# Kernel tuning notes

Hardware: AMD Instinct MI355X
Metric: run time of the kernel (lower is better)

Reference implementation:

```python
import jax, jax.numpy as jnp
import numpy as np
import math

NUM_CONVS = 4
GN_GROUPS = 32
GN_EPS = 1e-5
FPN_STRIDES = (8, 16, 32, 64, 128)
PRIOR_PROB = 0.01


def conv3x3(x, w, b):
    # x: [N,C,H,W], w: [O,I,3,3]
    y = jax.lax.conv_general_dilated(
        x, w, window_strides=(1, 1), padding='SAME',
        dimension_numbers=('NCHW', 'OIHW', 'NCHW'))
    return y + b[None, :, None, None]


def group_norm(x, gamma, beta):
    n, c, h, w = x.shape
    xg = x.reshape(n, GN_GROUPS, c // GN_GROUPS, h, w)
    mean = xg.mean(axis=(2, 3, 4), keepdims=True)
    var = xg.var(axis=(2, 3, 4), keepdims=True)
    xn = ((xg - mean) * jax.lax.rsqrt(var + GN_EPS)).reshape(n, c, h, w)
    return xn * gamma[None, :, None, None] + beta[None, :, None, None]


def subnet(x, ws, bs, gws, gbs):
    # NUM_CONVS x (conv3x3 -> GN -> ReLU)
    for i in range(NUM_CONVS):
        x = jax.nn.relu(group_norm(conv3x3(x, ws[i], bs[i]), gws[i], gbs[i]))
    return x


def permute_to_N_HWA_K(x, k):
    n = x.shape[0]
    return x.transpose(0, 2, 3, 1).reshape(n, -1, k)


def setup_inputs() -> dict:
    key = jax.random.key(0)
    ks = jax.random.split(key, 16)
    C, K = 256, 80
    feats = {
        'p3': jax.random.normal(ks[0], (1, C, 80, 80), jnp.float32),
        'p4': jax.random.normal(ks[1], (1, C, 40, 40), jnp.float32),
        'p5': jax.random.normal(ks[2], (1, C, 20, 20), jnp.float32),
        'p6': jax.random.normal(ks[3], (1, C, 10, 10), jnp.float32),
        'p7': jax.random.normal(ks[4], (1, C, 5, 5), jnp.float32),
    }
    std = 0.01
    bias_value = -math.log((1 - PRIOR_PROB) / PRIOR_PROB)
    params = {
        'cls_w': std * jax.random.normal(ks[5], (NUM_CONVS, C, C, 3, 3), jnp.float32),
        'cls_b': jnp.zeros((NUM_CONVS, C), jnp.float32),
        'cls_gn_w': jnp.ones((NUM_CONVS, C), jnp.float32),
        'cls_gn_b': jnp.zeros((NUM_CONVS, C), jnp.float32),
        'box_w': std * jax.random.normal(ks[6], (NUM_CONVS, C, C, 3, 3), jnp.float32),
        'box_b': jnp.zeros((NUM_CONVS, C), jnp.float32),
        'box_gn_w': jnp.ones((NUM_CONVS, C), jnp.float32),
        'box_gn_b': jnp.zeros((NUM_CONVS, C), jnp.float32),
        'score_w': std * jax.random.normal(ks[7], (K, C, 3, 3), jnp.float32),
        'score_b': jnp.full((K,), bias_value, jnp.float32),
        'pred_w': std * jax.random.normal(ks[8], (4, C, 3, 3), jnp.float32),
        'pred_b': jnp.zeros((4,), jnp.float32),
        'iou_w': std * jax.random.normal(ks[9], (1, C, 3, 3), jnp.float32),
        'iou_b': jnp.zeros((1,), jnp.float32),
        'scales': jnp.ones((5,), jnp.float32),
    }
    return {**feats, **params}


def reference(p3, p4, p5, p6, p7,
              cls_w, cls_b, cls_gn_w, cls_gn_b,
              box_w, box_b, box_gn_w, box_gn_b,
              score_w, score_b, pred_w, pred_b, iou_w, iou_b, scales):
    features = [p3, p4, p5, p6, p7]
    logits, bbox_reg, ious = [], [], []
    for l, feat in enumerate(features):
        c = subnet(feat, cls_w, cls_b, cls_gn_w, cls_gn_b)
        b = subnet(feat, box_w, box_b, box_gn_w, box_gn_b)
        logit = conv3x3(c, score_w, score_b)          # [N,80,H,W]
        iou = conv3x3(b, iou_w, iou_b)                # [N,1,H,W]
        bp = conv3x3(b, pred_w, pred_b) * scales[l]   # Scale module
        # norm_reg_targets=True branch
        reg = jax.nn.relu(bp) * FPN_STRIDES[l]        # [N,4,H,W]
        logits.append(permute_to_N_HWA_K(logit, 80))
        bbox_reg.append(permute_to_N_HWA_K(reg, 4))
        ious.append(permute_to_N_HWA_K(iou, 1))
    box_cls = jnp.concatenate(logits, axis=1)    # [N, sumHW, 80]
    box_delta = jnp.concatenate(bbox_reg, axis=1)  # [N, sumHW, 4]
    box_iou = jnp.concatenate(ious, axis=1)      # [N, sumHW, 1]
    # pack into one array for a single output: [N, sumHW, 85]
    return jnp.concatenate([box_cls, box_delta, box_iou], axis=-1)
```

## Files before the change

kernel.cpp:

```cpp
#include <hip/hip_runtime.h>

typedef unsigned short u16;
typedef __attribute__((ext_vector_type(8))) short bf16x8;
typedef __attribute__((ext_vector_type(4))) float f32x4;

#define NLEV 5
#define CCH 256
#define KTOT 2304
#define P_TOT 8525
#define PP_TOT 9165
#define PLS (PP_TOT*64)
#define HSTR 11776

__constant__ int   c_HW[NLEV]     = {6400, 1600, 400, 100, 25};
__constant__ int   c_W[NLEV]      = {80, 40, 20, 10, 5};
__constant__ int   c_off[NLEV]    = {0, 6400, 8000, 8400, 8500};
__constant__ int   c_poff[NLEV]   = {0, 6724, 8488, 8972, 9116};
__constant__ int   c_tls[NLEV+1]  = {0, 50, 65, 71, 73, 74};
__constant__ int   c_ntx[NLEV]    = {5, 3, 2, 1, 1};
__constant__ float c_stridef[NLEV]= {8.f, 16.f, 32.f, 64.f, 128.f};

__device__ __forceinline__ u16 f2bf(float f){
  union { float f; unsigned u; } v; v.f = f;
  unsigned r = v.u + 0x7fffu + ((v.u >> 16) & 1u);
  return (u16)(r >> 16);
}

__device__ __forceinline__ void g2l16(const u16* g, u16* l, int lane){
#if defined(__has_builtin)
#if __has_builtin(__builtin_amdgcn_global_load_lds)
  __builtin_amdgcn_global_load_lds(
      (const __attribute__((address_space(1))) unsigned int*)g,
      (__attribute__((address_space(3))) unsigned int*)l, 16, 0, 0);
  return;
#endif
#endif
  *(uint4*)(l + lane*8) = *(const uint4*)g;
}

#define WAIT_VM4   0x0F74
#define WAIT_VM10  0x0F7A
#define WAIT_VM0   0x0F70
#define WAIT_LGKM0 0xC07F

template<int MODE>
__global__ __launch_bounds__(256, 2) void gemm_conv(
    const u16* __restrict__ Xc, const u16* __restrict__ Xb,
    const u16* __restrict__ Wc, const u16* __restrict__ Wb,
    const float* __restrict__ bc, const float* __restrict__ bb,
    float* __restrict__ Yc, float* __restrict__ Yb,
    float* __restrict__ stats,
    const float* __restrict__ predb, const float* __restrict__ ioub,
    const float* __restrict__ scales, float* __restrict__ out)
{
  __shared__ u16 hB[2*HSTR];
  __shared__ u16 sA[4][2][2048];
  __shared__ float sstat[16][2];

  const int ptile = blockIdx.x;
  const int mtile = (MODE == 0) ? blockIdx.y : 0;
  const int br = blockIdx.z;
  int lv = 0;
  #pragma unroll
  for (int i = 1; i < NLEV; i++) if (ptile >= c_tls[i]) lv = i;
  const int tidx = ptile - c_tls[lv];
  const int ntx = c_ntx[lv];
  const int ty0 = (tidx / ntx) * 8, tx0 = (tidx - (tidx / ntx) * ntx) * 16;
  const int W = c_W[lv], wrow2 = W + 2;

  const int tid = threadIdx.x, wv = tid >> 6, ln = tid & 63;
  const int quad = ln >> 4, l15 = ln & 15;

  const u16* __restrict__ X  = br ? Xb : Xc;
  const u16* __restrict__ WA = br ? Wb : Wc;

  const int ASTR = (MODE == 0) ? 16384 : 8192;
  const u16* abase = WA +
      (size_t)(((MODE == 0) ? mtile*16 : 0) + wv*4) * 512 + ln*8;

  const u16* hptr[6]; int hslab[6];
  #pragma unroll
  for (int i = 0; i < 6; i++) {
    int j = wv + 4*i;
    if (j > 22) j -= 4;
    hslab[i] = j;
    const int item = j*64 + ln;
    int hp = item >> 3; if (hp >= 180) hp -= 180;
    const int g = item & 7;
    const int hy = hp / 18, hx = hp - hy*18;
    const int prow = c_poff[lv] + (ty0 + hy)*wrow2 + tx0 + hx;
    hptr[i] = X + (size_t)prow*64 + ((g ^ (hp & 7)) << 3);
  }

  auto stageH = [&](int plane) {
    u16* dst = &hB[(plane & 1) * HSTR];
    const size_t cof = (size_t)plane * PLS;
    #pragma unroll
    for (int i = 0; i < 6; i++)
      g2l16(hptr[i] + cof, dst + hslab[i]*512, ln);
  };
  auto stageA = [&](int s, int b) {
    const u16* as = abase + (size_t)s * ASTR;
    u16* da = &sA[wv][b][0];
    #pragma unroll
    for (int j = 0; j < 4; j++) g2l16(as + j*512, da + j*512, ln);
  };

  f32x4 acc[2][8];
  #pragma unroll
  for (int i = 0; i < 2; i++)
    #pragma unroll
    for (int j = 0; j < 8; j++) acc[i][j] = (f32x4){0.f, 0.f, 0.f, 0.f};

  if (MODE == 0 && tid < 32) sstat[tid >> 1][tid & 1] = 0.f;

  stageH(0);
  stageH(1);
  stageA(0, 0);
  stageA(4, 1);
  __syncthreads();

  int cc = 0, tap = 0;
  #pragma unroll 1
  for (int t = 0; t < 36; t++) {
    if (t == 10 || t == 19) __builtin_amdgcn_s_waitcnt(WAIT_VM10);
    else if (t == 35)       __builtin_amdgcn_s_waitcnt(WAIT_VM0);
    else                    __builtin_amdgcn_s_waitcnt(WAIT_VM4);
    if (tap == 0 && cc > 0) {
      __builtin_amdgcn_sched_barrier(0);
      __builtin_amdgcn_s_barrier();
      __builtin_amdgcn_sched_barrier(0);
      if (cc < 3) stageH(cc + 1);
    }
    const u16* myA = &sA[wv][t & 1][0];
    const u16* hpl = &hB[(cc & 1) * HSTR];
    const int dh = tap / 3, dw = tap - dh*3;
    bf16x8 af[2][2], bf[2][8];
    #pragma unroll
    for (int sub = 0; sub < 2; sub++) {
      const int q = sub*4 + quad;
      const int swzA = (q ^ (l15 & 7)) * 8;
      #pragma unroll
      for (int mt = 0; mt < 2; mt++)
        af[sub][mt] = *(const bf16x8*)&myA[(mt*16 + l15)*64 + swzA];
      #pragma unroll
      for (int nt = 0; nt < 8; nt++) {
        const int hp = (nt + dh)*18 + l15 + dw;
        bf[sub][nt] = *(const bf16x8*)&hpl[hp*64 + ((q ^ (hp & 7)) << 3)];
      }
    }
    __builtin_amdgcn_s_waitcnt(WAIT_LGKM0);
    if (t < 34) {
      int tap2 = tap + 2, cc2 = cc;
      if (tap2 >= 9) { tap2 -= 9; cc2++; }
      stageA(tap2*4 + cc2, t & 1);
    }
    #pragma unroll
    for (int sub = 0; sub < 2; sub++)
      #pragma unroll
      for (int mt = 0; mt < 2; mt++)
        #pragma unroll
        for (int nt = 0; nt < 8; nt++)
          acc[mt][nt] = __builtin_amdgcn_mfma_f32_16x16x32_bf16(
              af[sub][mt], bf[sub][nt], acc[mt][nt], 0, 0, 0);
    if (++tap == 9) { tap = 0; cc++; }
  }

  const int gx = tx0 + l15;
  if (MODE == 0) {
    const float* __restrict__ bias = br ? bb : bc;
    float* __restrict__ Y = br ? Yb : Yc;
    #pragma unroll
    for (int mt = 0; mt < 2; mt++) {
      const int mloc = wv*32 + mt*16 + quad*4;
      const int mrow = mtile*128 + mloc;
      const f32x4 bv = *(const f32x4*)&bias[mrow];
      float s = 0.f, sq = 0.f;
      #pragma unroll
      for (int nt = 0; nt < 8; nt++) {
        const int gy = ty0 + nt;
        f32x4 v = acc[mt][nt] + bv;
        if (gy < W && gx < W) {
          const size_t n = (size_t)(c_off[lv] + gy*W + gx);
          *(f32x4*)&Y[n*CCH + mrow] = v;
          #pragma unroll
          for (int r = 0; r < 4; r++) { s += v[r]; sq += v[r]*v[r]; }
        }
      }
      #pragma unroll
      for (int o = 1; o < 16; o <<= 1) { s += __shfl_xor(s, o); sq += __shfl_xor(sq, o); }
      if (l15 == 0) {
        const int g = mloc >> 3;
        atomicAdd(&sstat[g][0], s);
        atomicAdd(&sstat[g][1], sq);
      }
    }
    __syncthreads();
    if (tid < 32) {
      const int g = tid >> 1, c = tid & 1;
      atomicAdd(&stats[((br*NLEV + lv)*32 + mtile*16 + g)*2 + c], sstat[g][c]);
    }
  } else {
    const float scl = scales[lv];
    const float stf = c_stridef[lv];
    #pragma unroll
    for (int mt = 0; mt < 2; mt++) {
      const int mr0 = wv*32 + mt*16 + quad*4;
      if (mr0 >= 85) continue;
      #pragma unroll
      for (int nt = 0; nt < 8; nt++) {
        const int gy = ty0 + nt;
        if (gy >= W || gx >= W) continue;
        const size_t n = (size_t)(c_off[lv] + gy*W + gx);
        const f32x4 v = acc[mt][nt];
        #pragma unroll
        for (int r = 0; r < 4; r++) {
          const int m = mr0 + r;
          if (br == 0) {
            if (m < 80) out[n*85 + m] = v[r] + bc[m];
          } else {
            if (m < 4) {
              const float t = (v[r] + predb[m]) * scl;
              out[n*85 + 80 + m] = fmaxf(t, 0.f) * stf;
            } else if (m == 4) {
              out[n*85 + 84] = v[r] + ioub[0];
            }
          }
        }
      }
    }
  }
}

__global__ __launch_bounds__(256) void gn_relu(
    const float* __restrict__ Yc, const float* __restrict__ Yb,
    const float* __restrict__ stats,
    const float* __restrict__ gwc, const float* __restrict__ gbc,
    const float* __restrict__ gwb, const float* __restrict__ gbb,
    u16* __restrict__ Xc, u16* __restrict__ Xb)
{
  const int t = blockIdx.x * 256 + threadIdx.x;
  if (t >= 2 * P_TOT * 32) return;
  const int br = t / (P_TOT * 32);
  const int r  = t - br * (P_TOT * 32);
  const int pg = r >> 5;
  const int c0 = (r & 31) << 3;
  int lv = 0;
  #pragma unroll
  for (int i = 1; i < NLEV; i++) if (pg >= c_off[i]) lv = i;
  const int pl = pg - c_off[lv];
  const int Wl = c_W[lv];
  const int g = c0 >> 3;
  const float* st = &stats[(((size_t)br*NLEV + lv)*32 + g)*2];
  const float cnt = 8.f * (float)c_HW[lv];
  const float mean = st[0] / cnt;
  const float var  = st[1] / cnt - mean*mean;
  const float rstd = rsqrtf(var + 1e-5f);
  const float* Y  = br ? Yb : Yc;
  const float* gw = br ? gwb : gwc;
  const float* gb = br ? gbb : gbc;
  u16* X = br ? Xb : Xc;
  const float* y = &Y[(size_t)pg*CCH + c0];
  const int h = pl / Wl, wi = pl - h*Wl;
  const size_t pidx = (size_t)(c_poff[lv] + (h+1)*(Wl+2) + (wi+1));
  union { u16 u[8]; uint4 v; } pk;
  #pragma unroll
  for (int i = 0; i < 8; i++) {
    const float v = (y[i] - mean)*rstd*gw[c0+i] + gb[c0+i];
    pk.u[i] = f2bf(fmaxf(v, 0.f));
  }
  *(uint4*)&X[(size_t)(c0 >> 6)*PLS + pidx*64 + (c0 & 63)] = pk.v;
}

__global__ __launch_bounds__(256) void feat2bf(
    const float* __restrict__ p3, const float* __restrict__ p4,
    const float* __restrict__ p5, const float* __restrict__ p6,
    const float* __restrict__ p7, u16* __restrict__ X)
{
  const int t = blockIdx.x * 256 + threadIdx.x;
  if (t >= P_TOT * 32) return;
  const int pg = t >> 5, c0 = (t & 31) << 3;
  int lv = 0;
  #pragma unroll
  for (int i = 1; i < NLEV; i++) if (pg >= c_off[i]) lv = i;
  const int pl = pg - c_off[lv];
  const float* src = lv==0 ? p3 : lv==1 ? p4 : lv==2 ? p5 : lv==3 ? p6 : p7;
  const int HW = c_HW[lv], Wl = c_W[lv];
  const int h = pl / Wl, wi = pl - h*Wl;
  const size_t pidx = (size_t)(c_poff[lv] + (h+1)*(Wl+2) + (wi+1));
  union { u16 u[8]; uint4 v; } pk;
  #pragma unroll
  for (int i = 0; i < 8; i++)
    pk.u[i] = f2bf(src[(size_t)(c0+i)*HW + pl]);
  *(uint4*)&X[(size_t)(c0 >> 6)*PLS + pidx*64 + (c0 & 63)] = pk.v;
}

__global__ __launch_bounds__(256) void wconv(
    const float* __restrict__ cw, const float* __restrict__ bw,
    u16* __restrict__ Wc, u16* __restrict__ Wb)
{
  const size_t N = (size_t)4*256*KTOT;
  const size_t t = (size_t)blockIdx.x * 256 + threadIdx.x;
  if (t >= 2*N) return;
  const float* src = (t < N) ? cw : bw;
  u16* dst = (t < N) ? Wc : Wb;
  const size_t i = (t < N) ? t : t - N;
  const size_t lc = i / KTOT;
  const int kk = (int)(i - lc*KTOT);
  const int l = (int)(lc >> 8), co = (int)(lc & 255);
  const int tap = kk >> 8, ci = kk & 255;
  const int s = kk >> 6, kl = kk & 63;
  const int r = co & 7, p = (kl >> 3) ^ r;
  const size_t d = (size_t)l*589824 +
      ((size_t)((s*32 + (co >> 3))*64 + r*8 + p))*8 + (kl & 7);
  dst[d] = f2bf(src[(lc*256 + ci)*9 + tap]);
}

__global__ __launch_bounds__(256) void hconv(
    const float* __restrict__ sw, const float* __restrict__ pw,
    const float* __restrict__ iw, u16* __restrict__ Whc, u16* __restrict__ Whb)
{
  const int N = 128 * KTOT;
  const int t = blockIdx.x * 256 + threadIdx.x;
  if (t >= 2*N) return;
  const int i = (t < N) ? t : t - N;
  const int co = i / KTOT, kk = i - co*KTOT;
  const int tap = kk >> 8, ci = kk & 255;
  const int s = kk >> 6, kl = kk & 63;
  const int r = co & 7, p = (kl >> 3) ^ r;
  const size_t d = ((size_t)((s*16 + (co >> 3))*64 + r*8 + p))*8 + (kl & 7);
  float v = 0.f;
  if (t < N) {
    if (co < 80) v = sw[(co*256 + ci)*9 + tap];
    Whc[d] = f2bf(v);
  } else {
    if (co < 4)       v = pw[(co*256 + ci)*9 + tap];
    else if (co == 4) v = iw[ci*9 + tap];
    Whb[d] = f2bf(v);
  }
}

extern "C" void kernel_launch(void* const* d_in, const int* in_sizes, int n_in,
                              void* d_out, int out_size, void* d_ws, size_t ws_size,
                              hipStream_t stream)
{
  const float* p3      = (const float*)d_in[0];
  const float* p4      = (const float*)d_in[1];
  const float* p5      = (const float*)d_in[2];
  const float* p6      = (const float*)d_in[3];
  const float* p7      = (const float*)d_in[4];
  const float* cls_w   = (const float*)d_in[5];
  const float* cls_b   = (const float*)d_in[6];
  const float* cls_gw  = (const float*)d_in[7];
  const float* cls_gb  = (const float*)d_in[8];
  const float* box_w   = (const float*)d_in[9];
  const float* box_b   = (const float*)d_in[10];
  const float* box_gw  = (const float*)d_in[11];
  const float* box_gb  = (const float*)d_in[12];
  const float* score_w = (const float*)d_in[13];
  const float* score_b = (const float*)d_in[14];
  const float* pred_w  = (const float*)d_in[15];
  const float* pred_b  = (const float*)d_in[16];
  const float* iou_w   = (const float*)d_in[17];
  const float* iou_b   = (const float*)d_in[18];
  const float* scales  = (const float*)d_in[19];
  float* out = (float*)d_out;

  char* w = (char*)d_ws;
  size_t o = 0;
  auto alloc = [&](size_t b) { void* p = w + o; o += (b + 255) & ~(size_t)255; return p; };
  u16*   XF = (u16*)alloc((size_t)PP_TOT*CCH*2);
  u16*   XC = (u16*)alloc((size_t)PP_TOT*CCH*2);
  u16*   XB = (u16*)alloc((size_t)PP_TOT*CCH*2);
  float* ST = (float*)alloc((size_t)4*2*NLEV*32*2*4);
  u16*  WRC = (u16*)alloc((size_t)4*256*KTOT*2);
  u16*  WRB = (u16*)alloc((size_t)4*256*KTOT*2);
  u16*  WHC = (u16*)alloc((size_t)128*KTOT*2);
  u16*  WHB = (u16*)alloc((size_t)128*KTOT*2);
  float* YC = (float*)alloc((size_t)P_TOT*CCH*4);
  float* YB = (float*)alloc((size_t)P_TOT*CCH*4);

  hipMemsetAsync(XF, 0, (size_t)3*PP_TOT*CCH*2 + (size_t)4*2*NLEV*32*2*4, stream);

  wconv<<<dim3((unsigned)(((size_t)2*4*256*KTOT + 255)/256)), 256, 0, stream>>>(cls_w, box_w, WRC, WRB);
  hconv<<<dim3((2*128*KTOT + 255)/256), 256, 0, stream>>>(score_w, pred_w, iou_w, WHC, WHB);
  feat2bf<<<dim3((P_TOT*32 + 255)/256), 256, 0, stream>>>(p3, p4, p5, p6, p7, XF);

  const u16* xci = XF; const u16* xbi = XF;
  for (int l = 0; l < 4; l++) {
    float* STl = ST + (size_t)l*2*NLEV*32*2;
    gemm_conv<0><<<dim3(74, 2, 2), 256, 0, stream>>>(
        xci, xbi, WRC + (size_t)l*589824, WRB + (size_t)l*589824,
        cls_b + l*256, box_b + l*256, YC, YB, STl,
        nullptr, nullptr, nullptr, nullptr);
    gn_relu<<<dim3((2*P_TOT*32 + 255)/256), 256, 0, stream>>>(
        YC, YB, STl, cls_gw + l*256, cls_gb + l*256, box_gw + l*256, box_gb + l*256,
        XC, XB);
    xci = XC; xbi = XB;
  }
  gemm_conv<1><<<dim3(74, 1, 2), 256, 0, stream>>>(
      xci, xbi, WHC, WHB, score_b, nullptr, nullptr, nullptr, nullptr,
      pred_b, iou_b, scales, out);
}
```

Baseline: 354.8 us.

## Load weight fragments directly into registers and stage input halo through registers

Weights are repacked into MFMA fragment order so each lane loads its A operands straight from global memory into a triple-buffered register set, dropping the LDS weight buffers and their barriers. The input halo staging switches from async global-to-LDS loads to a register prefetch issued two taps early and written to LDS at the plane boundary. The main loop is fully unrolled with compiler-managed waits in place of hand-tuned waitcnt values. This removes LDS traffic for weights but raises register pressure and exposes global load latency on the A path.

```diff
diff --git a/kernel.cpp b/kernel.cpp
--- a/kernel.cpp
+++ b/kernel.cpp
@@ -25,23 +25,6 @@
   unsigned r = v.u + 0x7fffu + ((v.u >> 16) & 1u);
   return (u16)(r >> 16);
 }
-
-__device__ __forceinline__ void g2l16(const u16* g, u16* l, int lane){
-#if defined(__has_builtin)
-#if __has_builtin(__builtin_amdgcn_global_load_lds)
-  __builtin_amdgcn_global_load_lds(
-      (const __attribute__((address_space(1))) unsigned int*)g,
-      (__attribute__((address_space(3))) unsigned int*)l, 16, 0, 0);
-  return;
-#endif
-#endif
-  *(uint4*)(l + lane*8) = *(const uint4*)g;
-}
-
-#define WAIT_VM4   0x0F74
-#define WAIT_VM10  0x0F7A
-#define WAIT_VM0   0x0F70
-#define WAIT_LGKM0 0xC07F
 
 template<int MODE>
 __global__ __launch_bounds__(256, 2) void gemm_conv(
@@ -54,7 +37,6 @@
     const float* __restrict__ scales, float* __restrict__ out)
 {
   __shared__ u16 hB[2*HSTR];
-  __shared__ u16 sA[4][2][2048];
   __shared__ float sstat[16][2];
 
   const int ptile = blockIdx.x;
@@ -74,9 +56,13 @@
   const u16* __restrict__ X  = br ? Xb : Xc;
   const u16* __restrict__ WA = br ? Wb : Wc;
 
-  const int ASTR = (MODE == 0) ? 16384 : 8192;
-  const u16* abase = WA +
-      (size_t)(((MODE == 0) ? mtile*16 : 0) + wv*4) * 512 + ln*8;
+  const u16* ap[2][2];
+  const u16* abase = WA + (size_t)((MODE == 0) ? mtile*294912 : 0);
+  #pragma unroll
+  for (int mt = 0; mt < 2; mt++)
+    #pragma unroll
+    for (int sub = 0; sub < 2; sub++)
+      ap[mt][sub] = abase + (((wv*2 + mt)*2 + sub)*512) + ln*8;
 
   const u16* hptr[6]; int hslab[6];
   #pragma unroll
@@ -92,18 +78,26 @@
     hptr[i] = X + (size_t)prow*64 + ((g ^ (hp & 7)) << 3);
   }
 
-  auto stageH = [&](int plane) {
+  uint4 hreg[6];
+  auto hload = [&](int plane) {
+    #pragma unroll
+    for (int i = 0; i < 6; i++)
+      hreg[i] = *(const uint4*)(hptr[i] + (size_t)plane * PLS);
+  };
+  auto hwrite = [&](int plane) {
     u16* dst = &hB[(plane & 1) * HSTR];
-    const size_t cof = (size_t)plane * PLS;
     #pragma unroll
     for (int i = 0; i < 6; i++)
-      g2l16(hptr[i] + cof, dst + hslab[i]*512, ln);
+      *(uint4*)&dst[hslab[i]*512 + ln*8] = hreg[i];
   };
-  auto stageA = [&](int s, int b) {
-    const u16* as = abase + (size_t)s * ASTR;
-    u16* da = &sA[wv][b][0];
-    #pragma unroll
-    for (int j = 0; j < 4; j++) g2l16(as + j*512, da + j*512, ln);
+
+  bf16x8 aB[3][2][2];
+  auto aload = [&](int s, int b) {
+    #pragma unroll
+    for (int mt = 0; mt < 2; mt++)
+      #pragma unroll
+      for (int sub = 0; sub < 2; sub++)
+        aB[b][mt][sub] = *(const bf16x8*)(ap[mt][sub] + (size_t)s*8192);
   };
 
   f32x4 acc[2][8];
@@ -114,56 +108,39 @@
 
   if (MODE == 0 && tid < 32) sstat[tid >> 1][tid & 1] = 0.f;
 
-  stageH(0);
-  stageH(1);
-  stageA(0, 0);
-  stageA(4, 1);
+  hload(0); hwrite(0);
+  hload(1); hwrite(1);
+  aload(0, 0);
+  aload(1, 1);
   __syncthreads();
 
-  int cc = 0, tap = 0;
-  #pragma unroll 1
+  #pragma unroll
   for (int t = 0; t < 36; t++) {
-    if (t == 10 || t == 19) __builtin_amdgcn_s_waitcnt(WAIT_VM10);
-    else if (t == 35)       __builtin_amdgcn_s_waitcnt(WAIT_VM0);
-    else                    __builtin_amdgcn_s_waitcnt(WAIT_VM4);
+    const int cc = t / 9, tap = t - cc*9;
     if (tap == 0 && cc > 0) {
-      __builtin_amdgcn_sched_barrier(0);
-      __builtin_amdgcn_s_barrier();
-      __builtin_amdgcn_sched_barrier(0);
-      if (cc < 3) stageH(cc + 1);
-    }
-    const u16* myA = &sA[wv][t & 1][0];
+      __syncthreads();
+      if (cc < 3) hwrite(cc + 1);
+    }
+    if (tap == 7 && cc < 2) hload(cc + 2);
+    if (t < 34) aload(t + 2, (t + 2) % 3);
     const u16* hpl = &hB[(cc & 1) * HSTR];
     const int dh = tap / 3, dw = tap - dh*3;
-    bf16x8 af[2][2], bf[2][8];
     #pragma unroll
     for (int sub = 0; sub < 2; sub++) {
       const int q = sub*4 + quad;
-      const int swzA = (q ^ (l15 & 7)) * 8;
-      #pragma unroll
-      for (int mt = 0; mt < 2; mt++)
-        af[sub][mt] = *(const bf16x8*)&myA[(mt*16 + l15)*64 + swzA];
+      bf16x8 bf[8];
       #pragma unroll
       for (int nt = 0; nt < 8; nt++) {
         const int hp = (nt + dh)*18 + l15 + dw;
-        bf[sub][nt] = *(const bf16x8*)&hpl[hp*64 + ((q ^ (hp & 7)) << 3)];
+        bf[nt] = *(const bf16x8*)&hpl[hp*64 + ((q ^ (hp & 7)) << 3)];
       }
-    }
-    __builtin_amdgcn_s_waitcnt(WAIT_LGKM0);
-    if (t < 34) {
-      int tap2 = tap + 2, cc2 = cc;
-      if (tap2 >= 9) { tap2 -= 9; cc2++; }
-      stageA(tap2*4 + cc2, t & 1);
-    }
-    #pragma unroll
-    for (int sub = 0; sub < 2; sub++)
       #pragma unroll
       for (int mt = 0; mt < 2; mt++)
         #pragma unroll
         for (int nt = 0; nt < 8; nt++)
           acc[mt][nt] = __builtin_amdgcn_mfma_f32_16x16x32_bf16(
-              af[sub][mt], bf[sub][nt], acc[mt][nt], 0, 0, 0);
-    if (++tap == 9) { tap = 0; cc++; }
+              aB[t % 3][mt][sub], bf[nt], acc[mt][nt], 0, 0, 0);
+    }
   }
 
   const int gx = tx0 + l15;
@@ -309,10 +286,13 @@
   const int kk = (int)(i - lc*KTOT);
   const int l = (int)(lc >> 8), co = (int)(lc & 255);
   const int tap = kk >> 8, ci = kk & 255;
-  const int s = kk >> 6, kl = kk & 63;
-  const int r = co & 7, p = (kl >> 3) ^ r;
-  const size_t d = (size_t)l*589824 +
-      ((size_t)((s*32 + (co >> 3))*64 + r*8 + p))*8 + (kl & 7);
+  const int s = (ci >> 6)*9 + tap;
+  const int kl = ci & 63;
+  const int sub = kl >> 5, quad = (kl >> 3) & 3, j = kl & 7;
+  const int ln = quad*16 + (co & 15);
+  const int mtl = (co >> 4) & 7, comtile = co >> 7;
+  const size_t d = (size_t)l*589824 + (size_t)comtile*294912 +
+      ((size_t)((s*8 + mtl)*2 + sub))*512 + ln*8 + j;
   dst[d] = f2bf(src[(lc*256 + ci)*9 + tap]);
 }
 
@@ -326,9 +306,12 @@
   const int i = (t < N) ? t : t - N;
   const int co = i / KTOT, kk = i - co*KTOT;
   const int tap = kk >> 8, ci = kk & 255;
-  const int s = kk >> 6, kl = kk & 63;
-  const int r = co & 7, p = (kl >> 3) ^ r;
-  const size_t d = ((size_t)((s*16 + (co >> 3))*64 + r*8 + p))*8 + (kl & 7);
+  const int s = (ci >> 6)*9 + tap;
+  const int kl = ci & 63;
+  const int sub = kl >> 5, quad = (kl >> 3) & 3, j = kl & 7;
+  const int ln = quad*16 + (co & 15);
+  const int mtl = co >> 4;
+  const size_t d = ((size_t)((s*8 + mtl)*2 + sub))*512 + ln*8 + j;
   float v = 0.f;
   if (t < N) {
     if (co < 80) v = sw[(co*256 + ci)*9 + tap];
```

Result: slower. 560.2 us (+57.9%).

## Fuse subnet conv and GroupNorm layers into one cooperative persistent kernel

Applied to the files above, without the earlier changes.

Replaces the per-layer sequence of conv GEMM and GN+ReLU launches, plus the head conv, with a single cooperative kernel of 296 blocks. Grid-wide syncs separate the conv, stats and normalize phases. This is meant to remove kernel launch gaps and tail effects between the nine dependent launches. In exchange it adds grid barrier costs and requires the blocks to be co-resident, with the old multi-launch path kept as a fallback if the cooperative launch fails.

```diff
diff --git a/kernel.cpp b/kernel.cpp
--- a/kernel.cpp
+++ b/kernel.cpp
@@ -1,4 +1,6 @@
 #include <hip/hip_runtime.h>
+#include <hip/hip_cooperative_groups.h>
+namespace cg = cooperative_groups;
 
 typedef unsigned short u16;
 typedef __attribute__((ext_vector_type(8))) short bf16x8;
@@ -11,6 +13,7 @@
 #define PP_TOT 9165
 #define PLS (PP_TOT*64)
 #define HSTR 11776
+#define NBLK 296
 
 __constant__ int   c_HW[NLEV]     = {6400, 1600, 400, 100, 25};
 __constant__ int   c_W[NLEV]      = {80, 40, 20, 10, 5};
@@ -42,6 +45,341 @@
 #define WAIT_VM10  0x0F7A
 #define WAIT_VM0   0x0F70
 #define WAIT_LGKM0 0xC07F
+
+struct MegaParams {
+  const u16 *XF;
+  u16 *XC, *XB;
+  const u16 *WRC, *WRB, *WHC, *WHB;
+  float *YC, *YB, *ST;
+  const float *cls_b, *box_b, *cls_gw, *cls_gb, *box_gw, *box_gb;
+  const float *score_b, *pred_b, *iou_b, *scales;
+  float *out;
+};
+
+__global__ __launch_bounds__(256, 2) void fcos_mega(MegaParams P)
+{
+  __shared__ u16 hB[2*HSTR];
+  __shared__ u16 sA[4][2][2048];
+  __shared__ float sstat[16][2];
+  cg::grid_group grid = cg::this_grid();
+
+  const int bid = blockIdx.x;
+  const int tid = threadIdx.x, wv = tid >> 6, ln = tid & 63;
+  const int quad = ln >> 4, l15 = ln & 15;
+
+  const int ptile = bid % 74;
+  const int mtile = (bid / 74) & 1;
+  const int br    = bid / 148;
+  int lv = 0;
+  #pragma unroll
+  for (int i = 1; i < NLEV; i++) if (ptile >= c_tls[i]) lv = i;
+  const int tidx = ptile - c_tls[lv];
+  const int ntx = c_ntx[lv];
+  const int ty0 = (tidx / ntx) * 8, tx0 = (tidx - (tidx / ntx) * ntx) * 16;
+  const int W = c_W[lv], wrow2 = W + 2;
+  const int gx = tx0 + l15;
+  const int aoff = (mtile*16 + wv*4)*512 + ln*8;
+
+  int hoff[6], hslab[6];
+  #pragma unroll
+  for (int i = 0; i < 6; i++) {
+    int j = wv + 4*i;
+    if (j > 22) j -= 4;
+    hslab[i] = j;
+    const int item = j*64 + ln;
+    int hp = item >> 3; if (hp >= 180) hp -= 180;
+    const int g = item & 7;
+    const int hy = hp / 18, hx = hp - hy*18;
+    const int prow = c_poff[lv] + (ty0 + hy)*wrow2 + tx0 + hx;
+    hoff[i] = prow*64 + ((g ^ (hp & 7)) << 3);
+  }
+
+  #pragma unroll 1
+  for (int l = 0; l < 4; l++) {
+    const u16* X = (l == 0) ? P.XF : (br ? (const u16*)P.XB : (const u16*)P.XC);
+    const u16* WA = (br ? P.WRB : P.WRC) + (size_t)l*589824;
+    const float* bias = (br ? P.box_b : P.cls_b) + l*256;
+    float* Y = br ? P.YB : P.YC;
+    float* STl = P.ST + (size_t)l*2*NLEV*32*2;
+
+    auto stageH = [&](int plane) {
+      u16* dst = &hB[(plane & 1) * HSTR];
+      const size_t cof = (size_t)plane * PLS;
+      #pragma unroll
+      for (int i = 0; i < 6; i++)
+        g2l16(X + hoff[i] + cof, dst + hslab[i]*512, ln);
+    };
+    auto stageA = [&](int s, int b) {
+      const u16* as = WA + aoff + (size_t)s * 16384;
+      u16* da = &sA[wv][b][0];
+      #pragma unroll
+      for (int j = 0; j < 4; j++) g2l16(as + j*512, da + j*512, ln);
+    };
+
+    f32x4 acc[2][8];
+    #pragma unroll
+    for (int i = 0; i < 2; i++)
+      #pragma unroll
+      for (int j = 0; j < 8; j++) acc[i][j] = (f32x4){0.f, 0.f, 0.f, 0.f};
+
+    if (tid < 32) sstat[tid >> 1][tid & 1] = 0.f;
+
+    stageH(0);
+    stageH(1);
+    stageA(0, 0);
+    stageA(4, 1);
+    __syncthreads();
+
+    int cc = 0, tap = 0;
+    #pragma unroll 1
+    for (int t = 0; t < 36; t++) {
+      if (t == 10 || t == 19) __builtin_amdgcn_s_waitcnt(WAIT_VM10);
+      else if (t == 35)       __builtin_amdgcn_s_waitcnt(WAIT_VM0);
+      else                    __builtin_amdgcn_s_waitcnt(WAIT_VM4);
+      if (tap == 0 && cc > 0) {
+        __builtin_amdgcn_sched_barrier(0);
+        __builtin_amdgcn_s_barrier();
+        __builtin_amdgcn_sched_barrier(0);
+        if (cc < 3) stageH(cc + 1);
+      }
+      const u16* myA = &sA[wv][t & 1][0];
+      const u16* hpl = &hB[(cc & 1) * HSTR];
+      const int dh = tap / 3, dw = tap - dh*3;
+      bf16x8 af[2][2], bf[2][8];
+      #pragma unroll
+      for (int sub = 0; sub < 2; sub++) {
+        const int q = sub*4 + quad;
+        const int swzA = (q ^ (l15 & 7)) * 8;
+        #pragma unroll
+        for (int mt = 0; mt < 2; mt++)
+          af[sub][mt] = *(const bf16x8*)&myA[(mt*16 + l15)*64 + swzA];
+        #pragma unroll
+        for (int nt = 0; nt < 8; nt++) {
+          const int hp = (nt + dh)*18 + l15 + dw;
+          bf[sub][nt] = *(const bf16x8*)&hpl[hp*64 + ((q ^ (hp & 7)) << 3)];
+        }
+      }
+      __builtin_amdgcn_s_waitcnt(WAIT_LGKM0);
+      if (t < 34) {
+        int tap2 = tap + 2, cc2 = cc;
+        if (tap2 >= 9) { tap2 -= 9; cc2++; }
+        stageA(tap2*4 + cc2, t & 1);
+      }
+      #pragma unroll
+      for (int sub = 0; sub < 2; sub++)
+        #pragma unroll
+        for (int mt = 0; mt < 2; mt++)
+          #pragma unroll
+          for (int nt = 0; nt < 8; nt++)
+            acc[mt][nt] = __builtin_amdgcn_mfma_f32_16x16x32_bf16(
+                af[sub][mt], bf[sub][nt], acc[mt][nt], 0, 0, 0);
+      if (++tap == 9) { tap = 0; cc++; }
+    }
+
+    #pragma unroll
+    for (int mt = 0; mt < 2; mt++) {
+      const int mloc = wv*32 + mt*16 + quad*4;
+      const int mrow = mtile*128 + mloc;
+      const f32x4 bv = *(const f32x4*)&bias[mrow];
+      float s = 0.f, sq = 0.f;
+      #pragma unroll
+      for (int nt = 0; nt < 8; nt++) {
+        const int gy = ty0 + nt;
+        f32x4 v = acc[mt][nt] + bv;
+        if (gy < W && gx < W) {
+          const size_t n = (size_t)(c_off[lv] + gy*W + gx);
+          *(f32x4*)&Y[n*CCH + mrow] = v;
+          #pragma unroll
+          for (int r = 0; r < 4; r++) { s += v[r]; sq += v[r]*v[r]; }
+        }
+      }
+      #pragma unroll
+      for (int o = 1; o < 16; o <<= 1) { s += __shfl_xor(s, o); sq += __shfl_xor(sq, o); }
+      if (l15 == 0) {
+        const int g = mloc >> 3;
+        atomicAdd(&sstat[g][0], s);
+        atomicAdd(&sstat[g][1], sq);
+      }
+    }
+    __syncthreads();
+    if (tid < 32) {
+      const int g = tid >> 1, c = tid & 1;
+      atomicAdd(&STl[((br*NLEV + lv)*32 + mtile*16 + g)*2 + c], sstat[g][c]);
+    }
+
+    __threadfence();
+    grid.sync();
+    __threadfence();
+
+    for (int t0 = bid*256 + tid; t0 < 2*P_TOT*32; t0 += NBLK*256) {
+      const int gbr = t0 / (P_TOT * 32);
+      const int r  = t0 - gbr * (P_TOT * 32);
+      const int pg = r >> 5;
+      const int c0 = (r & 31) << 3;
+      int glv = 0;
+      #pragma unroll
+      for (int i = 1; i < NLEV; i++) if (pg >= c_off[i]) glv = i;
+      const int pl = pg - c_off[glv];
+      const int Wl = c_W[glv];
+      const int gg = c0 >> 3;
+      const float* st = &STl[((gbr*NLEV + glv)*32 + gg)*2];
+      const float cnt = 8.f * (float)c_HW[glv];
+      const float mean = st[0] / cnt;
+      const float var  = st[1] / cnt - mean*mean;
+      const float rstd = rsqrtf(var + 1e-5f);
+      const float* Yg = gbr ? P.YB : P.YC;
+      const float* gw = (gbr ? P.box_gw : P.cls_gw) + l*256;
+      const float* gb = (gbr ? P.box_gb : P.cls_gb) + l*256;
+      u16* Xo = gbr ? P.XB : P.XC;
+      const float* y = &Yg[(size_t)pg*CCH + c0];
+      const int h = pl / Wl, wi = pl - h*Wl;
+      const size_t pidx = (size_t)(c_poff[glv] + (h+1)*(Wl+2) + (wi+1));
+      union { u16 u[8]; uint4 v; } pk;
+      #pragma unroll
+      for (int i = 0; i < 8; i++) {
+        const float v = (y[i] - mean)*rstd*gw[c0+i] + gb[c0+i];
+        pk.u[i] = f2bf(fmaxf(v, 0.f));
+      }
+      *(uint4*)&Xo[(size_t)(c0 >> 6)*PLS + pidx*64 + (c0 & 63)] = pk.v;
+    }
+
+    __threadfence();
+    grid.sync();
+    __threadfence();
+  }
+
+  if (bid >= 148) return;
+  {
+    const int hbr = bid / 74, hpt = bid % 74;
+    int lv2 = 0;
+    #pragma unroll
+    for (int i = 1; i < NLEV; i++) if (hpt >= c_tls[i]) lv2 = i;
+    const int tix = hpt - c_tls[lv2];
+    const int nt2 = c_ntx[lv2];
+    const int hy0 = (tix / nt2) * 8, hx0 = (tix - (tix / nt2) * nt2) * 16;
+    const int W2 = c_W[lv2], wr2 = W2 + 2;
+    const int gx2 = hx0 + l15;
+
+    const u16* X = hbr ? (const u16*)P.XB : (const u16*)P.XC;
+    const u16* WA = hbr ? P.WHB : P.WHC;
+    const int aoff2 = (wv*4)*512 + ln*8;
+
+    int hoff2[6], hslab2[6];
+    #pragma unroll
+    for (int i = 0; i < 6; i++) {
+      int j = wv + 4*i;
+      if (j > 22) j -= 4;
+      hslab2[i] = j;
+      const int item = j*64 + ln;
+      int hp = item >> 3; if (hp >= 180) hp -= 180;
+      const int g = item & 7;
+      const int hy = hp / 18, hx = hp - hy*18;
+      const int prow = c_poff[lv2] + (hy0 + hy)*wr2 + hx0 + hx;
+      hoff2[i] = prow*64 + ((g ^ (hp & 7)) << 3);
+    }
+
+    auto stageH2 = [&](int plane) {
+      u16* dst = &hB[(plane & 1) * HSTR];
+      const size_t cof = (size_t)plane * PLS;
+      #pragma unroll
+      for (int i = 0; i < 6; i++)
+        g2l16(X + hoff2[i] + cof, dst + hslab2[i]*512, ln);
+    };
+    auto stageA2 = [&](int s, int b) {
+      const u16* as = WA + aoff2 + (size_t)s * 8192;
+      u16* da = &sA[wv][b][0];
+      #pragma unroll
+      for (int j = 0; j < 4; j++) g2l16(as + j*512, da + j*512, ln);
+    };
+
+    f32x4 acc[2][8];
+    #pragma unroll
+    for (int i = 0; i < 2; i++)
+      #pragma unroll
+      for (int j = 0; j < 8; j++) acc[i][j] = (f32x4){0.f, 0.f, 0.f, 0.f};
+
+    stageH2(0);
+    stageH2(1);
+    stageA2(0, 0);
+    stageA2(4, 1);
+    __syncthreads();
+
+    int cc = 0, tap = 0;
+    #pragma unroll 1
+    for (int t = 0; t < 36; t++) {
+      if (t == 10 || t == 19) __builtin_amdgcn_s_waitcnt(WAIT_VM10);
+      else if (t == 35)       __builtin_amdgcn_s_waitcnt(WAIT_VM0);
+      else                    __builtin_amdgcn_s_waitcnt(WAIT_VM4);
+      if (tap == 0 && cc > 0) {
+        __builtin_amdgcn_sched_barrier(0);
+        __builtin_amdgcn_s_barrier();
+        __builtin_amdgcn_sched_barrier(0);
+        if (cc < 3) stageH2(cc + 1);
+      }
+      const u16* myA = &sA[wv][t & 1][0];
+      const u16* hpl = &hB[(cc & 1) * HSTR];
+      const int dh = tap / 3, dw = tap - dh*3;
+      bf16x8 af[2][2], bf[2][8];
+      #pragma unroll
+      for (int sub = 0; sub < 2; sub++) {
+        const int q = sub*4 + quad;
+        const int swzA = (q ^ (l15 & 7)) * 8;
+        #pragma unroll
+        for (int mt = 0; mt < 2; mt++)
+          af[sub][mt] = *(const bf16x8*)&myA[(mt*16 + l15)*64 + swzA];
+        #pragma unroll
+        for (int nt = 0; nt < 8; nt++) {
+          const int hp = (nt + dh)*18 + l15 + dw;
+          bf[sub][nt] = *(const bf16x8*)&hpl[hp*64 + ((q ^ (hp & 7)) << 3)];
+        }
+      }
+      __builtin_amdgcn_s_waitcnt(WAIT_LGKM0);
+      if (t < 34) {
+        int tap2 = tap + 2, cc2 = cc;
+        if (tap2 >= 9) { tap2 -= 9; cc2++; }
+        stageA2(tap2*4 + cc2, t & 1);
+      }
+      #pragma unroll
+      for (int sub = 0; sub < 2; sub++)
+        #pragma unroll
+        for (int mt = 0; mt < 2; mt++)
+          #pragma unroll
+          for (int nt = 0; nt < 8; nt++)
+            acc[mt][nt] = __builtin_amdgcn_mfma_f32_16x16x32_bf16(
+                af[sub][mt], bf[sub][nt], acc[mt][nt], 0, 0, 0);
+      if (++tap == 9) { tap = 0; cc++; }
+    }
+
+    const float scl = P.scales[lv2];
+    const float stf = c_stridef[lv2];
+    #pragma unroll
+    for (int mt = 0; mt < 2; mt++) {
+      const int mr0 = wv*32 + mt*16 + quad*4;
+      if (mr0 >= 85) continue;
+      #pragma unroll
+      for (int nt = 0; nt < 8; nt++) {
+        const int gy = hy0 + nt;
+        if (gy >= W2 || gx2 >= W2) continue;
+        const size_t n = (size_t)(c_off[lv2] + gy*W2 + gx2);
+        const f32x4 v = acc[mt][nt];
+        #pragma unroll
+        for (int r = 0; r < 4; r++) {
+          const int m = mr0 + r;
+          if (hbr == 0) {
+            if (m < 80) P.out[n*85 + m] = v[r] + P.score_b[m];
+          } else {
+            if (m < 4) {
+              const float t = (v[r] + P.pred_b[m]) * scl;
+              P.out[n*85 + 80 + m] = fmaxf(t, 0.f) * stf;
+            } else if (m == 4) {
+              P.out[n*85 + 84] = v[r] + P.iou_b[0];
+            }
+          }
+        }
+      }
+    }
+  }
+}
 
 template<int MODE>
 __global__ __launch_bounds__(256, 2) void gemm_conv(
@@ -386,19 +724,34 @@
   hconv<<<dim3((2*128*KTOT + 255)/256), 256, 0, stream>>>(score_w, pred_w, iou_w, WHC, WHB);
   feat2bf<<<dim3((P_TOT*32 + 255)/256), 256, 0, stream>>>(p3, p4, p5, p6, p7, XF);
 
-  const u16* xci = XF; const u16* xbi = XF;
-  for (int l = 0; l < 4; l++) {
-    float* STl = ST + (size_t)l*2*NLEV*32*2;
-    gemm_conv<0><<<dim3(74, 2, 2), 256, 0, stream>>>(
-        xci, xbi, WRC + (size_t)l*589824, WRB + (size_t)l*589824,
-        cls_b + l*256, box_b + l*256, YC, YB, STl,
-        nullptr, nullptr, nullptr, nullptr);
-    gn_relu<<<dim3((2*P_TOT*32 + 255)/256), 256, 0, stream>>>(
-        YC, YB, STl, cls_gw + l*256, cls_gb + l*256, box_gw + l*256, box_gb + l*256,
-        XC, XB);
-    xci = XC; xbi = XB;
-  }
-  gemm_conv<1><<<dim3(74, 1, 2), 256, 0, stream>>>(
-      xci, xbi, WHC, WHB, score_b, nullptr, nullptr, nullptr, nullptr,
-      pred_b, iou_b, scales, out);
-}
+  MegaParams mp;
+  mp.XF = XF; mp.XC = XC; mp.XB = XB;
+  mp.WRC = WRC; mp.WRB = WRB; mp.WHC = WHC; mp.WHB = WHB;
+  mp.YC = YC; mp.YB = YB; mp.ST = ST;
+  mp.cls_b = cls_b; mp.box_b = box_b;
+  mp.cls_gw = cls_gw; mp.cls_gb = cls_gb;
+  mp.box_gw = box_gw; mp.box_gb = box_gb;
+  mp.score_b = score_b; mp.pred_b = pred_b; mp.iou_b = iou_b;
+  mp.scales = scales; mp.out = out;
+  void* kargs[] = { &mp };
+  hipError_t ce = hipLaunchCooperativeKernel((const void*)fcos_mega, dim3(NBLK),
+                                             dim3(256), kargs, 0, stream);
+  if (ce != hipSuccess) {
+    (void)hipGetLastError();
+    const u16* xci = XF; const u16* xbi = XF;
+    for (int l = 0; l < 4; l++) {
+      float* STl = ST + (size_t)l*2*NLEV*32*2;
+      gemm_conv<0><<<dim3(74, 2, 2), 256, 0, stream>>>(
+          xci, xbi, WRC + (size_t)l*589824, WRB + (size_t)l*589824,
+          cls_b + l*256, box_b + l*256, YC, YB, STl,
+          nullptr, nullptr, nullptr, nullptr);
+      gn_relu<<<dim3((2*P_TOT*32 + 255)/256), 256, 0, stream>>>(
+          YC, YB, STl, cls_gw + l*256, cls_gb + l*256, box_gw + l*256, box_gb + l*256,
+          XC, XB);
+      xci = XC; xbi = XB;
+    }
+    gemm_conv<1><<<dim3(74, 1, 2), 256, 0, stream>>>(
+        xci, xbi, WHC, WHB, score_b, nullptr, nullptr, nullptr, nullptr,
+        pred_b, iou_b, scales, out);
+  }
+}
```

Measured after the change: 1.100 ms. +210.1%, slower.

## Fuse GroupNorm+ReLU into next conv's input staging via per-channel coefficients

Applied to the files above, without the earlier changes.

Replaces the standalone gn_relu pass, which materialised a padded bf16 activation buffer, with a tiny gn_coef kernel that computes per-channel scale/shift. The following conv kernel then reads the fp32 conv output directly, applies the affine and ReLU, converts to bf16 in registers and writes the result to LDS, with zeros for halo pixels. This removes one full write and read pass per layer. The cost is that halo staging now goes through register loads, doubling fp32 read traffic, and uses full __syncthreads instead of async global-to-LDS loads, which may reduce overlap inside the conv. Output buffers are ping-ponged because each conv reads the previous layer's raw output.

```diff
diff --git a/kernel.cpp b/kernel.cpp
--- a/kernel.cpp
+++ b/kernel.cpp
@@ -43,9 +43,11 @@
 #define WAIT_VM0   0x0F70
 #define WAIT_LGKM0 0xC07F
 
-template<int MODE>
+template<int MODE, int SRC>
 __global__ __launch_bounds__(256, 2) void gemm_conv(
     const u16* __restrict__ Xc, const u16* __restrict__ Xb,
+    const float* __restrict__ Ypc, const float* __restrict__ Ypb,
+    const float* __restrict__ CFS, const float* __restrict__ CFH,
     const u16* __restrict__ Wc, const u16* __restrict__ Wb,
     const float* __restrict__ bc, const float* __restrict__ bb,
     float* __restrict__ Yc, float* __restrict__ Yb,
@@ -71,14 +73,17 @@
   const int tid = threadIdx.x, wv = tid >> 6, ln = tid & 63;
   const int quad = ln >> 4, l15 = ln & 15;
 
-  const u16* __restrict__ X  = br ? Xb : Xc;
+  const u16* X = br ? Xb : Xc;
+  const float* Yp = br ? Ypb : Ypc;
   const u16* __restrict__ WA = br ? Wb : Wc;
 
   const int ASTR = (MODE == 0) ? 16384 : 8192;
   const u16* abase = WA +
       (size_t)(((MODE == 0) ? mtile*16 : 0) + wv*4) * 512 + ln*8;
 
-  const u16* hptr[6]; int hslab[6];
+  const u16* hptr[6];
+  int noffs[6], cfo[6]; bool oobf[6];
+  int hslab[6];
   #pragma unroll
   for (int i = 0; i < 6; i++) {
     int j = wv + 4*i;
@@ -87,17 +92,52 @@
     const int item = j*64 + ln;
     int hp = item >> 3; if (hp >= 180) hp -= 180;
     const int g = item & 7;
+    const int gsw8 = (g ^ (hp & 7)) * 8;
     const int hy = hp / 18, hx = hp - hy*18;
-    const int prow = c_poff[lv] + (ty0 + hy)*wrow2 + tx0 + hx;
-    hptr[i] = X + (size_t)prow*64 + ((g ^ (hp & 7)) << 3);
-  }
-
+    if (SRC == 0) {
+      const int prow = c_poff[lv] + (ty0 + hy)*wrow2 + tx0 + hx;
+      hptr[i] = X + (size_t)prow*64 + gsw8;
+    } else {
+      const int y = ty0 + hy - 1, x = tx0 + hx - 1;
+      oobf[i] = (y < 0) | (y >= W) | (x < 0) | (x >= W);
+      const int n = oobf[i] ? 0 : (c_off[lv] + y*W + x);
+      noffs[i] = n*256 + gsw8;
+      cfo[i]   = (br*NLEV + lv)*256 + gsw8;
+    }
+  }
+
+  uint4 hreg[6];
   auto stageH = [&](int plane) {
     u16* dst = &hB[(plane & 1) * HSTR];
     const size_t cof = (size_t)plane * PLS;
     #pragma unroll
     for (int i = 0; i < 6; i++)
       g2l16(hptr[i] + cof, dst + hslab[i]*512, ln);
+  };
+  auto hloadN = [&](int cc) {
+    #pragma unroll
+    for (int i = 0; i < 6; i++) {
+      if (oobf[i]) { hreg[i] = (uint4){0,0,0,0}; continue; }
+      const float* p = Yp + noffs[i] + cc*64;
+      const f32x4 a0 = *(const f32x4*)p;
+      const f32x4 a1 = *(const f32x4*)(p + 4);
+      const float* cs = CFS + cfo[i] + cc*64;
+      const float* ch = CFH + cfo[i] + cc*64;
+      const f32x4 s0 = *(const f32x4*)cs, s1 = *(const f32x4*)(cs + 4);
+      const f32x4 h0 = *(const f32x4*)ch, h1 = *(const f32x4*)(ch + 4);
+      union { u16 u[8]; uint4 v; } pk;
+      #pragma unroll
+      for (int r = 0; r < 4; r++) pk.u[r]     = f2bf(fmaxf(a0[r]*s0[r] + h0[r], 0.f));
+      #pragma unroll
+      for (int r = 0; r < 4; r++) pk.u[4 + r] = f2bf(fmaxf(a1[r]*s1[r] + h1[r], 0.f));
+      hreg[i] = pk.v;
+    }
+  };
+  auto hwriteN = [&](int slot) {
+    u16* dst = &hB[slot * HSTR];
+    #pragma unroll
+    for (int i = 0; i < 6; i++)
+      *(uint4*)&dst[hslab[i]*512 + ln*8] = hreg[i];
   };
   auto stageA = [&](int s, int b) {
     const u16* as = abase + (size_t)s * ASTR;
@@ -114,8 +154,13 @@
 
   if (MODE == 0 && tid < 32) sstat[tid >> 1][tid & 1] = 0.f;
 
-  stageH(0);
-  stageH(1);
+  if (SRC == 0) {
+    stageH(0);
+    stageH(1);
+  } else {
+    hloadN(0); hwriteN(0);
+    hloadN(1); hwriteN(1);
+  }
   stageA(0, 0);
   stageA(4, 1);
   __syncthreads();
@@ -123,14 +168,19 @@
   int cc = 0, tap = 0;
   #pragma unroll 1
   for (int t = 0; t < 36; t++) {
-    if (t == 10 || t == 19) __builtin_amdgcn_s_waitcnt(WAIT_VM10);
-    else if (t == 35)       __builtin_amdgcn_s_waitcnt(WAIT_VM0);
-    else                    __builtin_amdgcn_s_waitcnt(WAIT_VM4);
+    if (SRC == 0 && (t == 10 || t == 19)) __builtin_amdgcn_s_waitcnt(WAIT_VM10);
+    else if (t == 35)                     __builtin_amdgcn_s_waitcnt(WAIT_VM0);
+    else                                  __builtin_amdgcn_s_waitcnt(WAIT_VM4);
     if (tap == 0 && cc > 0) {
-      __builtin_amdgcn_sched_barrier(0);
-      __builtin_amdgcn_s_barrier();
-      __builtin_amdgcn_sched_barrier(0);
-      if (cc < 3) stageH(cc + 1);
+      if (SRC == 0) {
+        __builtin_amdgcn_sched_barrier(0);
+        __builtin_amdgcn_s_barrier();
+        __builtin_amdgcn_sched_barrier(0);
+        if (cc < 3) stageH(cc + 1);
+      } else {
+        __syncthreads();
+        if (cc < 3) hwriteN((cc + 1) & 1);
+      }
     }
     const u16* myA = &sA[wv][t & 1][0];
     const u16* hpl = &hB[(cc & 1) * HSTR];
@@ -150,6 +200,7 @@
       }
     }
     __builtin_amdgcn_s_waitcnt(WAIT_LGKM0);
+    if (SRC == 1 && tap == 7 && cc < 2) hloadN(cc + 2);
     if (t < 34) {
       int tap2 = tap + 2, cc2 = cc;
       if (tap2 >= 9) { tap2 -= 9; cc2++; }
@@ -220,8 +271,8 @@
             if (m < 80) out[n*85 + m] = v[r] + bc[m];
           } else {
             if (m < 4) {
-              const float t = (v[r] + predb[m]) * scl;
-              out[n*85 + 80 + m] = fmaxf(t, 0.f) * stf;
+              const float t2 = (v[r] + predb[m]) * scl;
+              out[n*85 + 80 + m] = fmaxf(t2, 0.f) * stf;
             } else if (m == 4) {
               out[n*85 + 84] = v[r] + ioub[0];
             }
@@ -232,44 +283,27 @@
   }
 }
 
-__global__ __launch_bounds__(256) void gn_relu(
-    const float* __restrict__ Yc, const float* __restrict__ Yb,
-    const float* __restrict__ stats,
-    const float* __restrict__ gwc, const float* __restrict__ gbc,
-    const float* __restrict__ gwb, const float* __restrict__ gbb,
-    u16* __restrict__ Xc, u16* __restrict__ Xb)
+__global__ __launch_bounds__(256) void gn_coef(
+    const float* __restrict__ ST, const float* __restrict__ gwc,
+    const float* __restrict__ gbc, const float* __restrict__ gwb,
+    const float* __restrict__ gbb,
+    float* __restrict__ CFS, float* __restrict__ CFH)
 {
   const int t = blockIdx.x * 256 + threadIdx.x;
-  if (t >= 2 * P_TOT * 32) return;
-  const int br = t / (P_TOT * 32);
-  const int r  = t - br * (P_TOT * 32);
-  const int pg = r >> 5;
-  const int c0 = (r & 31) << 3;
-  int lv = 0;
-  #pragma unroll
-  for (int i = 1; i < NLEV; i++) if (pg >= c_off[i]) lv = i;
-  const int pl = pg - c_off[lv];
-  const int Wl = c_W[lv];
-  const int g = c0 >> 3;
-  const float* st = &stats[(((size_t)br*NLEV + lv)*32 + g)*2];
+  if (t >= 2*NLEV*256) return;
+  const int br = t / (NLEV*256);
+  const int r  = t - br*(NLEV*256);
+  const int lv = r >> 8, c = r & 255, g = c >> 3;
+  const float* st = &ST[((br*NLEV + lv)*32 + g)*2];
   const float cnt = 8.f * (float)c_HW[lv];
   const float mean = st[0] / cnt;
   const float var  = st[1] / cnt - mean*mean;
   const float rstd = rsqrtf(var + 1e-5f);
-  const float* Y  = br ? Yb : Yc;
   const float* gw = br ? gwb : gwc;
   const float* gb = br ? gbb : gbc;
-  u16* X = br ? Xb : Xc;
-  const float* y = &Y[(size_t)pg*CCH + c0];
-  const int h = pl / Wl, wi = pl - h*Wl;
-  const size_t pidx = (size_t)(c_poff[lv] + (h+1)*(Wl+2) + (wi+1));
-  union { u16 u[8]; uint4 v; } pk;
-  #pragma unroll
-  for (int i = 0; i < 8; i++) {
-    const float v = (y[i] - mean)*rstd*gw[c0+i] + gb[c0+i];
-    pk.u[i] = f2bf(fmaxf(v, 0.f));
-  }
-  *(uint4*)&X[(size_t)(c0 >> 6)*PLS + pidx*64 + (c0 & 63)] = pk.v;
+  const float s = rstd * gw[c];
+  CFS[t] = s;
+  CFH[t] = gb[c] - mean*s;
 }
 
 __global__ __launch_bounds__(256) void feat2bf(
@@ -370,35 +404,51 @@
   size_t o = 0;
   auto alloc = [&](size_t b) { void* p = w + o; o += (b + 255) & ~(size_t)255; return p; };
   u16*   XF = (u16*)alloc((size_t)PP_TOT*CCH*2);
-  u16*   XC = (u16*)alloc((size_t)PP_TOT*CCH*2);
-  u16*   XB = (u16*)alloc((size_t)PP_TOT*CCH*2);
   float* ST = (float*)alloc((size_t)4*2*NLEV*32*2*4);
   u16*  WRC = (u16*)alloc((size_t)4*256*KTOT*2);
   u16*  WRB = (u16*)alloc((size_t)4*256*KTOT*2);
   u16*  WHC = (u16*)alloc((size_t)128*KTOT*2);
   u16*  WHB = (u16*)alloc((size_t)128*KTOT*2);
-  float* YC = (float*)alloc((size_t)P_TOT*CCH*4);
-  float* YB = (float*)alloc((size_t)P_TOT*CCH*4);
-
-  hipMemsetAsync(XF, 0, (size_t)3*PP_TOT*CCH*2 + (size_t)4*2*NLEV*32*2*4, stream);
+  float* YPC = (float*)alloc((size_t)P_TOT*CCH*4);
+  float* YPB = (float*)alloc((size_t)P_TOT*CCH*4);
+  float* YQC = (float*)alloc((size_t)P_TOT*CCH*4);
+  float* YQB = (float*)alloc((size_t)P_TOT*CCH*4);
+  float* CFS = (float*)alloc((size_t)4*2*NLEV*256*4);
+  float* CFH = (float*)alloc((size_t)4*2*NLEV*256*4);
+
+  hipMemsetAsync(XF, 0, (size_t)PP_TOT*CCH*2 + (size_t)4*2*NLEV*32*2*4, stream);
 
   wconv<<<dim3((unsigned)(((size_t)2*4*256*KTOT + 255)/256)), 256, 0, stream>>>(cls_w, box_w, WRC, WRB);
   hconv<<<dim3((2*128*KTOT + 255)/256), 256, 0, stream>>>(score_w, pred_w, iou_w, WHC, WHB);
   feat2bf<<<dim3((P_TOT*32 + 255)/256), 256, 0, stream>>>(p3, p4, p5, p6, p7, XF);
 
-  const u16* xci = XF; const u16* xbi = XF;
-  for (int l = 0; l < 4; l++) {
+  const int CFN = 2*NLEV*256;
+  float* YoutC[4] = {YPC, YQC, YPC, YQC};
+  float* YoutB[4] = {YPB, YQB, YPB, YQB};
+
+  gemm_conv<0,0><<<dim3(74, 2, 2), 256, 0, stream>>>(
+      XF, XF, nullptr, nullptr, nullptr, nullptr,
+      WRC, WRB, cls_b, box_b, YoutC[0], YoutB[0], ST,
+      nullptr, nullptr, nullptr, nullptr);
+  gn_coef<<<dim3((CFN + 255)/256), 256, 0, stream>>>(
+      ST, cls_gw, cls_gb, box_gw, box_gb, CFS, CFH);
+
+  for (int l = 1; l < 4; l++) {
     float* STl = ST + (size_t)l*2*NLEV*32*2;
-    gemm_conv<0><<<dim3(74, 2, 2), 256, 0, stream>>>(
-        xci, xbi, WRC + (size_t)l*589824, WRB + (size_t)l*589824,
-        cls_b + l*256, box_b + l*256, YC, YB, STl,
+    gemm_conv<0,1><<<dim3(74, 2, 2), 256, 0, stream>>>(
+        nullptr, nullptr, YoutC[l-1], YoutB[l-1],
+        CFS + (size_t)(l-1)*CFN, CFH + (size_t)(l-1)*CFN,
+        WRC + (size_t)l*589824, WRB + (size_t)l*589824,
+        cls_b + l*256, box_b + l*256, YoutC[l], YoutB[l], STl,
         nullptr, nullptr, nullptr, nullptr);
-    gn_relu<<<dim3((2*P_TOT*32 + 255)/256), 256, 0, stream>>>(
-        YC, YB, STl, cls_gw + l*256, cls_gb + l*256, box_gw + l*256, box_gb + l*256,
-        XC, XB);
-    xci = XC; xbi = XB;
-  }
-  gemm_conv<1><<<dim3(74, 1, 2), 256, 0, stream>>>(
-      xci, xbi, WHC, WHB, score_b, nullptr, nullptr, nullptr, nullptr,
+    gn_coef<<<dim3((CFN + 255)/256), 256, 0, stream>>>(
+        STl, cls_gw + l*256, cls_gb + l*256, box_gw + l*256, box_gb + l*256,
+        CFS + (size_t)l*CFN, CFH + (size_t)l*CFN);
+  }
+
+  gemm_conv<1,1><<<dim3(74, 1, 2), 256, 0, stream>>>(
+      nullptr, nullptr, YoutC[3], YoutB[3],
+      CFS + (size_t)3*CFN, CFH + (size_t)3*CFN,
+      WHC, WHB, score_b, nullptr, nullptr, nullptr, nullptr,
       pred_b, iou_b, scales, out);
 }
```

Result: slower. 373.2 us (+5.2%).
